# Performance work log

Hardware: AMD Instinct MI355X
Metric: run time of the kernel (lower is better)

The kernel has to match this reference:

```python
import jax, jax.numpy as jnp
import numpy as np

SEQ, DM, NH, DH = 8192, 1024, 16, 64


def setup_inputs() -> dict:
    key = jax.random.key(0)
    k = jax.random.split(key, 8)
    return {
        "xs": jax.random.normal(k[0], (SEQ, DM), dtype=jnp.float32),
        "wq": jax.random.normal(k[1], (NH, DH, DM), dtype=jnp.float32),
        "wk": jax.random.normal(k[2], (NH, DH, DM), dtype=jnp.float32),
        "wv": jax.random.normal(k[3], (NH, DH, DM), dtype=jnp.float32),
        # MLP: Linear(NH*DH -> DM), gelu, Linear(DM -> NH*DH); eqx stores W as (out, in)
        "w1": jax.random.normal(k[4], (DM, NH * DH), dtype=jnp.float32) * 0.02,
        "b1": jnp.zeros((DM,), dtype=jnp.float32),
        "w2": jax.random.normal(k[5], (NH * DH, DM), dtype=jnp.float32) * 0.02,
        "b2": jnp.zeros((NH * DH,), dtype=jnp.float32),
    }


def _act(x):
    return jax.nn.elu(x) + 1.0


def reference(xs, wq, wk, wv, w1, b1, w2, b2):
    # project: (n_heads d_head d_model),(seq d_model) -> (seq n_heads d_head)
    q = jnp.einsum('hdm,sm->shd', wq, xs)
    k = jnp.einsum('hdm,sm->shd', wk, xs)
    v = jnp.einsum('hdm,sm->shd', wv, xs)

    def cell(state, qkv):
        s, z = state                      # s: (h, dk, dv), z: (h, dk)
        qt, kt, vt = qkv                  # each (h, d)
        kt = _act(kt)
        s = s + jnp.einsum('hk,hv->hkv', kt, vt)
        z = z + kt
        qa = _act(qt)
        # faithful to einops 'n_heads d_head_k d_head_v, n_heads d_head_q -> n_heads d_head_v'
        sq = jnp.einsum('hkv,hq->hv', s, qa)
        zq = jnp.einsum('hk,hq->h', z, qa)
        return (s, z), sq / zq[:, None]

    init = (jnp.zeros((NH, DH, DH), xs.dtype), jnp.zeros((NH, DH), xs.dtype))
    _, out = jax.lax.scan(cell, init, (q, k, v))   # out: (seq, h, d)
    out = out.reshape(SEQ, NH * DH)
    h = jax.nn.gelu(out @ w1.T + b1)
    return h @ w2.T + b2
```

## Files before the change

kernel.cpp:

```cpp
#include <hip/hip_runtime.h>
#include <hip/hip_bf16.h>

using bf16 = __hip_bfloat16;
typedef __attribute__((ext_vector_type(8))) short shortx8;
typedef __attribute__((ext_vector_type(4))) float f32x4;

#define SEQ 8192
#define DM 1024
#define NH 16
#define CHUNK 64
#define NC (SEQ / CHUNK)
#define NT (DM / 64)

__device__ __forceinline__ void load_lds16(const bf16* g, bf16* l) {
    __builtin_amdgcn_global_load_lds(
        (const __attribute__((address_space(1))) void*)g,
        (__attribute__((address_space(3))) void*)l, 16, 0, 0);
}

__device__ __forceinline__ unsigned ldsoff(const bf16* p) {
    return (unsigned)(unsigned long long)(__attribute__((address_space(3))) const void*)p;
}

__device__ __forceinline__ shortx8 dsr128(unsigned a) {
    shortx8 r;
    asm volatile("ds_read_b128 %0, %1" : "=v"(r) : "v"(a));
    return r;
}

__device__ __forceinline__ float bf2f(short s) {
    union { unsigned u; float f; } x;
    x.u = ((unsigned)(unsigned short)s) << 16;
    return x.f;
}

__global__ __launch_bounds__(256) void convert_all(const float* __restrict__ xs,
                                                   const float* __restrict__ wk,
                                                   const float* __restrict__ wv,
                                                   const float* __restrict__ w1,
                                                   const float* __restrict__ w2,
                                                   bf16* __restrict__ xsb,
                                                   bf16* __restrict__ wall) {
    const int b = blockIdx.x;
    const float* in;
    bf16* out;
    int blk;
    if (b < 8192) {
        in = xs; out = xsb; blk = b;
    } else {
        const int seg = (b - 8192) >> 10;
        blk = (b - 8192) & 1023;
        out = wall + (size_t)seg * DM * DM;
        if (seg == 0)      in = wk;
        else if (seg == 1) in = wv;
        else if (seg == 2) in = w1;
        else               in = w2;
    }
    size_t i = ((size_t)blk * 256 + threadIdx.x) * 4;
    float4 f = *(const float4*)(in + i);
    out[i + 0] = __float2bfloat16(f.x);
    out[i + 1] = __float2bfloat16(f.y);
    out[i + 2] = __float2bfloat16(f.z);
    out[i + 3] = __float2bfloat16(f.w);
}

__global__ __launch_bounds__(512, 2) void gemm256(const bf16* __restrict__ A,
                                                  const bf16* __restrict__ B,
                                                  void* __restrict__ Cv,
                                                  float* __restrict__ kappa,
                                                  int N) {
    __shared__ __align__(16) bf16 As[2][256][64];
    __shared__ __align__(16) bf16 Bs[2][256][64];

    const int tid = threadIdx.x;
    const int nwg = gridDim.x * gridDim.y;
    const int bid = blockIdx.x + blockIdx.y * gridDim.x;
    const int cpx = nwg >> 3;
    const int swz = (bid & 7) * cpx + (bid >> 3);
    const int ry  = swz % gridDim.y;
    const int rx  = swz / gridDim.y;
    const int bm  = ry * 256;
    const int bn  = rx * 256;

    const int wave = tid >> 6;
    const int lane = tid & 63;
    const int wr   = wave >> 2;
    const int wc   = wave & 3;
    const int quad = lane >> 4;
    const int m16  = lane & 15;
    const int r7   = m16 & 7;
    const int wr128 = wr * 128;
    const int wc64  = wc * 64;
    const int kp0 = ((quad ^ r7) * 8);
    const int kp1 = (((4 + quad) ^ r7) * 8);

    auto stageA = [&](int half, int kt) {
        #pragma unroll
        for (int it = 0; it < 2; ++it) {
            int s = it * 512 + tid;
            int row = s >> 3, pos = s & 7;
            int g = pos ^ (row & 7);
            load_lds16(A + (size_t)(bm + half * 128 + row) * DM + kt * 64 + g * 8,
                       &As[kt & 1][half * 128 + row][pos * 8]);
        }
    };
    auto stageB = [&](int half, int kt) {
        #pragma unroll
        for (int it = 0; it < 2; ++it) {
            int s = it * 512 + tid;
            int row = s >> 3, pos = s & 7;
            int g = pos ^ (row & 7);
            load_lds16(B + (size_t)(bn + half * 128 + row) * DM + kt * 64 + g * 8,
                       &Bs[kt & 1][half * 128 + row][pos * 8]);
        }
    };

    f32x4 acc[8][4];
    #pragma unroll
    for (int i = 0; i < 8; ++i)
        #pragma unroll
        for (int j = 0; j < 4; ++j)
            #pragma unroll
            for (int r = 0; r < 4; ++r) acc[i][j][r] = 0.f;

    stageA(0, 0); stageA(1, 0); stageB(0, 0); stageB(1, 0);
    stageB(0, 1); stageB(1, 1);
    asm volatile("s_waitcnt vmcnt(4)");
    __builtin_amdgcn_s_barrier();

    shortx8 af[4][2], blo[2][2], bhi[2][2];

    #pragma unroll 1
    for (int t = 0; t < NT; ++t) {
        const int sl = t & 1;
        if (t + 1 < NT) { stageA(0, t + 1); stageA(1, t + 1); }
        #pragma unroll
        for (int i = 0; i < 4; ++i) {
            af[i][0] = dsr128(ldsoff(&As[sl][wr128 + i * 16 + m16][kp0]));
            af[i][1] = dsr128(ldsoff(&As[sl][wr128 + i * 16 + m16][kp1]));
        }
        #pragma unroll
        for (int j = 0; j < 2; ++j) {
            blo[j][0] = dsr128(ldsoff(&Bs[sl][wc64 + j * 16 + m16][kp0]));
            blo[j][1] = dsr128(ldsoff(&Bs[sl][wc64 + j * 16 + m16][kp1]));
            bhi[j][0] = dsr128(ldsoff(&Bs[sl][wc64 + (j + 2) * 16 + m16][kp0]));
            bhi[j][1] = dsr128(ldsoff(&Bs[sl][wc64 + (j + 2) * 16 + m16][kp1]));
        }
        asm volatile("s_waitcnt lgkmcnt(0)");
        __builtin_amdgcn_sched_barrier(0);
        __builtin_amdgcn_s_setprio(1);
        #pragma unroll
        for (int i = 0; i < 4; ++i)
            #pragma unroll
            for (int j = 0; j < 2; ++j) {
                acc[i][j] = __builtin_amdgcn_mfma_f32_16x16x32_bf16(af[i][0], blo[j][0], acc[i][j], 0, 0, 0);
                acc[i][j] = __builtin_amdgcn_mfma_f32_16x16x32_bf16(af[i][1], blo[j][1], acc[i][j], 0, 0, 0);
                acc[i][j + 2] = __builtin_amdgcn_mfma_f32_16x16x32_bf16(af[i][0], bhi[j][0], acc[i][j + 2], 0, 0, 0);
                acc[i][j + 2] = __builtin_amdgcn_mfma_f32_16x16x32_bf16(af[i][1], bhi[j][1], acc[i][j + 2], 0, 0, 0);
            }
        __builtin_amdgcn_s_setprio(0);
        __builtin_amdgcn_s_barrier();

        if (t + 2 < NT) { stageB(0, t + 2); stageB(1, t + 2); }
        #pragma unroll
        for (int i = 0; i < 4; ++i) {
            af[i][0] = dsr128(ldsoff(&As[sl][wr128 + 64 + i * 16 + m16][kp0]));
            af[i][1] = dsr128(ldsoff(&As[sl][wr128 + 64 + i * 16 + m16][kp1]));
        }
        asm volatile("s_waitcnt lgkmcnt(0)");
        __builtin_amdgcn_sched_barrier(0);
        __builtin_amdgcn_s_setprio(1);
        #pragma unroll
        for (int i = 0; i < 4; ++i)
            #pragma unroll
            for (int j = 0; j < 2; ++j) {
                acc[4 + i][j] = __builtin_amdgcn_mfma_f32_16x16x32_bf16(af[i][0], blo[j][0], acc[4 + i][j], 0, 0, 0);
                acc[4 + i][j] = __builtin_amdgcn_mfma_f32_16x16x32_bf16(af[i][1], blo[j][1], acc[4 + i][j], 0, 0, 0);
                acc[4 + i][j + 2] = __builtin_amdgcn_mfma_f32_16x16x32_bf16(af[i][0], bhi[j][0], acc[4 + i][j + 2], 0, 0, 0);
                acc[4 + i][j + 2] = __builtin_amdgcn_mfma_f32_16x16x32_bf16(af[i][1], bhi[j][1], acc[4 + i][j + 2], 0, 0, 0);
            }
        __builtin_amdgcn_s_setprio(0);
        if (t + 2 < NT) {
            asm volatile("s_waitcnt vmcnt(4)");
        } else {
            asm volatile("s_waitcnt vmcnt(0)");
        }
        __builtin_amdgcn_s_barrier();
    }

    const int gcol0 = bn + wc64;
    if (gcol0 < DM) {
        const int h = gcol0 >> 6;
        #pragma unroll
        for (int i = 0; i < 8; ++i) {
            #pragma unroll
            for (int r = 0; r < 4; ++r) {
                float s = 0.f;
                #pragma unroll
                for (int j = 0; j < 4; ++j) {
                    float v = acc[i][j][r];
                    s += v > 0.f ? v + 1.f : __expf(v);
                }
                s += __shfl_xor(s, 1);
                s += __shfl_xor(s, 2);
                s += __shfl_xor(s, 4);
                s += __shfl_xor(s, 8);
                if (m16 == 0)
                    kappa[(size_t)h * SEQ + bm + wr128 + i * 16 + quad * 4 + r] = s;
            }
        }
    } else {
        bf16* vb = (bf16*)Cv;
        #pragma unroll
        for (int i = 0; i < 8; ++i) {
            int row0 = bm + wr128 + i * 16 + quad * 4;
            #pragma unroll
            for (int j = 0; j < 4; ++j) {
                int col = gcol0 - DM + j * 16 + m16;
                #pragma unroll
                for (int r = 0; r < 4; ++r)
                    vb[(size_t)(row0 + r) * DM + col] = __float2bfloat16(acc[i][j][r]);
            }
        }
    }
}

template <int MODE>
__global__ __launch_bounds__(512, 2) void gemm_mlp(const bf16* __restrict__ A,
                                                   const bf16* __restrict__ B,
                                                   void* __restrict__ Cv,
                                                   const float* __restrict__ bias,
                                                   int N) {
    __shared__ __align__(16) bf16 As[3][128][64];
    __shared__ __align__(16) bf16 Bs[2][256][64];

    const int tid = threadIdx.x;
    const int nwg = gridDim.x * gridDim.y;
    const int bid = blockIdx.x + blockIdx.y * gridDim.x;
    const int cpx = nwg >> 3;
    const int swz = (bid & 7) * cpx + (bid >> 3);
    const int ry  = swz % gridDim.y;
    const int rx  = swz / gridDim.y;
    const int bm  = ry * 128;
    const int bn  = rx * 256;

    const int wave = tid >> 6;
    const int lane = tid & 63;
    const int wr   = wave >> 2;
    const int wc   = wave & 3;
    const int quad = lane >> 4;
    const int m16  = lane & 15;
    const int r7   = m16 & 7;
    const int wr64 = wr * 64;
    const int wc64 = wc * 64;
    const int kp0 = ((quad ^ r7) * 8);
    const int kp1 = (((4 + quad) ^ r7) * 8);

    auto stageA = [&](int slot, int kt) {
        #pragma unroll
        for (int it = 0; it < 2; ++it) {
            int s = it * 512 + tid;
            int row = s >> 3, pos = s & 7;
            int g = pos ^ (row & 7);
            load_lds16(A + (size_t)(bm + row) * DM + kt * 64 + g * 8,
                       &As[slot][row][pos * 8]);
        }
    };
    auto stageB = [&](int half, int kt) {
        #pragma unroll
        for (int it = 0; it < 2; ++it) {
            int s = it * 512 + tid;
            int row = s >> 3, pos = s & 7;
            int g = pos ^ (row & 7);
            load_lds16(B + (size_t)(bn + half * 128 + row) * DM + kt * 64 + g * 8,
                       &Bs[kt & 1][half * 128 + row][pos * 8]);
        }
    };

    f32x4 acc[4][4];
    #pragma unroll
    for (int i = 0; i < 4; ++i)
        #pragma unroll
        for (int j = 0; j < 4; ++j)
            #pragma unroll
            for (int r = 0; r < 4; ++r) acc[i][j][r] = 0.f;

    stageA(0, 0); stageB(0, 0); stageB(1, 0);
    stageA(1, 1); stageB(0, 1); stageB(1, 1);
    asm volatile("s_waitcnt vmcnt(6)");
    __builtin_amdgcn_s_barrier();

    shortx8 af[4][2], bfr[4][2];

    int sl3 = 0;
    int st3 = 2;

    #pragma unroll 1
    for (int t = 0; t < NT; ++t) {
        const int slB = t & 1;
        if (t + 2 < NT) stageA(st3, t + 2);
        #pragma unroll
        for (int i = 0; i < 4; ++i) {
            af[i][0] = dsr128(ldsoff(&As[sl3][wr64 + i * 16 + m16][kp0]));
            af[i][1] = dsr128(ldsoff(&As[sl3][wr64 + i * 16 + m16][kp1]));
        }
        #pragma unroll
        for (int j = 0; j < 4; ++j) {
            bfr[j][0] = dsr128(ldsoff(&Bs[slB][wc64 + j * 16 + m16][kp0]));
            bfr[j][1] = dsr128(ldsoff(&Bs[slB][wc64 + j * 16 + m16][kp1]));
        }
        asm volatile("s_waitcnt lgkmcnt(0)");
        __builtin_amdgcn_sched_barrier(0);
        __builtin_amdgcn_s_setprio(1);
        #pragma unroll
        for (int i = 0; i < 4; ++i)
            #pragma unroll
            for (int j = 0; j < 2; ++j) {
                acc[i][j] = __builtin_amdgcn_mfma_f32_16x16x32_bf16(af[i][0], bfr[j][0], acc[i][j], 0, 0, 0);
                acc[i][j] = __builtin_amdgcn_mfma_f32_16x16x32_bf16(af[i][1], bfr[j][1], acc[i][j], 0, 0, 0);
            }
        __builtin_amdgcn_s_setprio(0);
        __builtin_amdgcn_s_barrier();

        if (t + 2 < NT) { stageB(0, t + 2); stageB(1, t + 2); }
        __builtin_amdgcn_s_setprio(1);
        #pragma unroll
        for (int i = 0; i < 4; ++i)
            #pragma unroll
            for (int j = 0; j < 2; ++j) {
                acc[i][j + 2] = __builtin_amdgcn_mfma_f32_16x16x32_bf16(af[i][0], bfr[j + 2][0], acc[i][j + 2], 0, 0, 0);
                acc[i][j + 2] = __builtin_amdgcn_mfma_f32_16x16x32_bf16(af[i][1], bfr[j + 2][1], acc[i][j + 2], 0, 0, 0);
            }
        __builtin_amdgcn_s_setprio(0);
        if (t + 2 < NT) {
            asm volatile("s_waitcnt vmcnt(6)");
        } else {
            asm volatile("s_waitcnt vmcnt(0)");
        }
        __builtin_amdgcn_s_barrier();
        sl3 = (sl3 == 2) ? 0 : sl3 + 1;
        st3 = (st3 == 2) ? 0 : st3 + 1;
    }

    #pragma unroll
    for (int i = 0; i < 4; ++i) {
        int row0 = bm + wr64 + i * 16 + quad * 4;
        #pragma unroll
        for (int j = 0; j < 4; ++j) {
            int col = bn + wc64 + j * 16 + m16;
            float bv = bias[col];
            #pragma unroll
            for (int r = 0; r < 4; ++r) {
                float v = acc[i][j][r] + bv;
                if (MODE == 2) {
                    float tt = tanhf(0.7978845608028654f * (v + 0.044715f * v * v * v));
                    ((bf16*)Cv)[(size_t)(row0 + r) * N + col] = __float2bfloat16(0.5f * v * (1.f + tt));
                } else {
                    ((float*)Cv)[(size_t)(row0 + r) * N + col] = v;
                }
            }
        }
    }
}

__global__ __launch_bounds__(256) void chunk_sums(const bf16* __restrict__ vb,
                                                  const float* __restrict__ kappa,
                                                  float* __restrict__ numbuf,
                                                  float* __restrict__ denbuf) {
    const int h = blockIdx.x, c = blockIdx.y;
    const int v = threadIdx.x & 63, tq = threadIdx.x >> 6;
    __shared__ float red[4][64];
    __shared__ float dred[4];
    float np = 0.f, dp = 0.f;
    #pragma unroll
    for (int i = 0; i < 16; ++i) {
        int t = c * 64 + tq * 16 + i;
        float kv = kappa[(size_t)h * SEQ + t];
        float vv = bf2f(((const short*)vb)[(size_t)t * DM + h * 64 + v]);
        np += kv * vv;
        dp += kv;
    }
    red[tq][v] = np;
    if (v == 0) dred[tq] = dp;
    __syncthreads();
    if (tq == 0) {
        float s = red[0][v] + red[1][v] + red[2][v] + red[3][v];
        numbuf[((size_t)h * NC + c) * 64 + v] = s;
        if (v == 0)
            denbuf[(size_t)h * NC + c] = dred[0] + dred[1] + dred[2] + dred[3];
    }
}

__global__ __launch_bounds__(256) void prefix_state(float* __restrict__ numbuf,
                                                    float* __restrict__ denbuf) {
    const int h = blockIdx.x;
    const int wave = threadIdx.x >> 6;
    const int d = threadIdx.x & 63;
    __shared__ float tot[4][64];
    __shared__ float dtot[4];

    float val[32], dval[32];
    const int c0 = wave * 32;
    #pragma unroll
    for (int i = 0; i < 32; ++i) {
        size_t idx = (size_t)h * NC + c0 + i;
        val[i]  = numbuf[idx * 64 + d];
        dval[i] = denbuf[idx];
    }
    float run = 0.f, drun = 0.f;
    #pragma unroll
    for (int i = 0; i < 32; ++i) {
        float t = val[i];  val[i]  = run;  run  += t;
        float dt = dval[i]; dval[i] = drun; drun += dt;
    }
    tot[wave][d] = run;
    if (d == 0) dtot[wave] = drun;
    __syncthreads();
    float off = 0.f, doff = 0.f;
    for (int w = 0; w < wave; ++w) { off += tot[w][d]; doff += dtot[w]; }
    #pragma unroll
    for (int i = 0; i < 32; ++i) {
        size_t idx = (size_t)h * NC + c0 + i;
        numbuf[idx * 64 + d] = val[i] + off;
        if (d == 0) denbuf[idx] = dval[i] + doff;
    }
}

__global__ __launch_bounds__(256) void chunk_out(const bf16* __restrict__ vb,
                                                 const float* __restrict__ kappa,
                                                 const float* __restrict__ numbuf,
                                                 const float* __restrict__ denbuf,
                                                 bf16* __restrict__ out) {
    const int h = blockIdx.x, c = blockIdx.y;
    __shared__ float Ksh[64];
    __shared__ float Vs[64][64];
    const int tid = threadIdx.x;

    #pragma unroll
    for (int it = 0; it < 2; ++it) {
        int s = it * 256 + tid;
        int r = s >> 3, d8 = (s & 7) * 8;
        shortx8 raw = *(const shortx8*)(vb + (size_t)(c * 64 + r) * DM + h * 64 + d8);
        #pragma unroll
        for (int e = 0; e < 8; ++e) Vs[r][d8 + e] = bf2f(raw[e]);
    }
    if (tid < 64) Ksh[tid] = kappa[(size_t)h * SEQ + c * 64 + tid];
    __syncthreads();

    const int t  = tid >> 2;
    const int v0 = (tid & 3) << 4;
    const size_t bidx = (size_t)h * NC + c;

    float den = denbuf[bidx];
    float num[16];
    #pragma unroll
    for (int jj = 0; jj < 4; ++jj) {
        float4 n4 = *(const float4*)&numbuf[bidx * 64 + v0 + jj * 4];
        num[jj * 4 + 0] = n4.x; num[jj * 4 + 1] = n4.y;
        num[jj * 4 + 2] = n4.z; num[jj * 4 + 3] = n4.w;
    }

    for (int i = 0; i <= t; ++i) {
        float s = Ksh[i];
        den += s;
        #pragma unroll
        for (int jj = 0; jj < 4; ++jj) {
            float4 v4 = *(const float4*)&Vs[i][v0 + jj * 4];
            num[jj * 4 + 0] += s * v4.x; num[jj * 4 + 1] += s * v4.y;
            num[jj * 4 + 2] += s * v4.z; num[jj * 4 + 3] += s * v4.w;
        }
    }

    const float inv = 1.0f / den;
    size_t og = (size_t)(c * 64 + t) * DM + h * 64 + v0;
    #pragma unroll
    for (int j = 0; j < 16; ++j) out[og + j] = __float2bfloat16(num[j] * inv);
}

extern "C" void kernel_launch(void* const* d_in, const int* in_sizes, int n_in,
                              void* d_out, int out_size, void* d_ws, size_t ws_size,
                              hipStream_t stream) {
    const float* xs = (const float*)d_in[0];
    const float* wk = (const float*)d_in[2];
    const float* wv = (const float*)d_in[3];
    const float* w1 = (const float*)d_in[4];
    const float* b1 = (const float*)d_in[5];
    const float* w2 = (const float*)d_in[6];
    const float* b2 = (const float*)d_in[7];
    float* y = (float*)d_out;

    char* base = (char*)d_ws;
    size_t off = 0;
    auto alloc = [&](size_t b) -> char* {
        char* p = base + off;
        off += (b + 255) & ~(size_t)255;
        return p;
    };

    const size_t NMAT = (size_t)SEQ * DM;
    const size_t NW   = (size_t)DM * DM;
    bf16*  xsb    = (bf16*)alloc(NMAT * 2);
    bf16*  wall   = (bf16*)alloc(4 * NW * 2);
    bf16*  w1b    = wall + 2 * NW;
    bf16*  w2b    = wall + 3 * NW;
    bf16*  vb     = (bf16*)alloc(NMAT * 2);
    float* kappa  = (float*)alloc((size_t)NH * SEQ * 4);
    float* numbuf = (float*)alloc((size_t)NH * NC * 64 * 4);
    float* denbuf = (float*)alloc((size_t)NH * NC * 4);
    bf16*  outb   = (bf16*)alloc(NMAT * 2);
    bf16*  hb     = (bf16*)alloc(NMAT * 2);

    convert_all<<<8192 + 4 * 1024, 256, 0, stream>>>(xs, wk, wv, w1, w2,
                                                     xsb, wall);

    gemm256<<<dim3(2048 / 256, SEQ / 256), 512, 0, stream>>>(
        xsb, wall, vb, kappa, 2048);

    chunk_sums<<<dim3(NH, NC), 256, 0, stream>>>(vb, kappa, numbuf, denbuf);
    prefix_state<<<NH, 256, 0, stream>>>(numbuf, denbuf);
    chunk_out<<<dim3(NH, NC), 256, 0, stream>>>(vb, kappa, numbuf, denbuf, outb);

    gemm_mlp<2><<<dim3(DM / 256, SEQ / 128), 512, 0, stream>>>(
        outb, w1b, hb, b1, DM);
    gemm_mlp<3><<<dim3(DM / 256, SEQ / 128), 512, 0, stream>>>(
        hb, w2b, y, b2, DM);
}
```

Baseline: 215.4 us.

## Replace quadratic intra-chunk output with per-lane sequential scan using wave shuffles

The chunk-output kernel is replaced. It used to stage V in LDS and have each thread redo a prefix sum over up to 64 rows (quadratic work). Now each wave owns one chunk and each lane owns one value column, so the running numerator and denominator are updated in one sequential pass, with kappa broadcast by shuffles. The chunk-sum kernel is reorganised the same way, one wave per chunk, with a shuffle reduction for the denominator, removing the LDS reductions and barriers. The new pattern does 2-byte strided loads and stores per lane across rows and a divide per step, and the launch uses a quarter as many blocks.

```diff
diff --git a/kernel.cpp b/kernel.cpp
--- a/kernel.cpp
+++ b/kernel.cpp
@@ -367,27 +367,51 @@
                                                   const float* __restrict__ kappa,
                                                   float* __restrict__ numbuf,
                                                   float* __restrict__ denbuf) {
-    const int h = blockIdx.x, c = blockIdx.y;
-    const int v = threadIdx.x & 63, tq = threadIdx.x >> 6;
-    __shared__ float red[4][64];
-    __shared__ float dred[4];
-    float np = 0.f, dp = 0.f;
-    #pragma unroll
-    for (int i = 0; i < 16; ++i) {
-        int t = c * 64 + tq * 16 + i;
-        float kv = kappa[(size_t)h * SEQ + t];
-        float vv = bf2f(((const short*)vb)[(size_t)t * DM + h * 64 + v]);
-        np += kv * vv;
-        dp += kv;
-    }
-    red[tq][v] = np;
-    if (v == 0) dred[tq] = dp;
-    __syncthreads();
-    if (tq == 0) {
-        float s = red[0][v] + red[1][v] + red[2][v] + red[3][v];
-        numbuf[((size_t)h * NC + c) * 64 + v] = s;
-        if (v == 0)
-            denbuf[(size_t)h * NC + c] = dred[0] + dred[1] + dred[2] + dred[3];
+    const int h = blockIdx.x;
+    const int c = blockIdx.y * 4 + (threadIdx.x >> 6);
+    const int v = threadIdx.x & 63;
+    const size_t bidx = (size_t)h * NC + c;
+
+    float kreg = kappa[(size_t)h * SEQ + c * 64 + v];
+    float num = 0.f;
+    const short* vrow = (const short*)vb + (size_t)(c * 64) * DM + h * 64 + v;
+    #pragma unroll 8
+    for (int t = 0; t < 64; ++t) {
+        float kt = __shfl(kreg, t);
+        num += kt * bf2f(vrow[0]);
+        vrow += DM;
+    }
+    numbuf[bidx * 64 + v] = num;
+    float d = kreg;
+    #pragma unroll
+    for (int off = 32; off > 0; off >>= 1) d += __shfl_xor(d, off);
+    if (v == 0) denbuf[bidx] = d;
+}
+
+__global__ __launch_bounds__(256) void chunk_scan(const bf16* __restrict__ vb,
+                                                  const float* __restrict__ kappa,
+                                                  const float* __restrict__ numbuf,
+                                                  const float* __restrict__ denbuf,
+                                                  bf16* __restrict__ out) {
+    const int h = blockIdx.x;
+    const int c = blockIdx.y * 4 + (threadIdx.x >> 6);
+    const int v = threadIdx.x & 63;
+    const size_t bidx = (size_t)h * NC + c;
+
+    float kreg = kappa[(size_t)h * SEQ + c * 64 + v];
+    float num = numbuf[bidx * 64 + v];
+    float den = denbuf[bidx];
+    const short* vrow = (const short*)vb + (size_t)(c * 64) * DM + h * 64 + v;
+    short* orow = (short*)out + (size_t)(c * 64) * DM + h * 64 + v;
+    #pragma unroll 8
+    for (int t = 0; t < 64; ++t) {
+        float kt = __shfl(kreg, t);
+        num += kt * bf2f(vrow[0]);
+        den += kt;
+        bf16 ob = __float2bfloat16(num / den);
+        orow[0] = *(const short*)&ob;
+        vrow += DM;
+        orow += DM;
     }
 }
 
@@ -424,57 +448,6 @@
         numbuf[idx * 64 + d] = val[i] + off;
         if (d == 0) denbuf[idx] = dval[i] + doff;
     }
-}
-
-__global__ __launch_bounds__(256) void chunk_out(const bf16* __restrict__ vb,
-                                                 const float* __restrict__ kappa,
-                                                 const float* __restrict__ numbuf,
-                                                 const float* __restrict__ denbuf,
-                                                 bf16* __restrict__ out) {
-    const int h = blockIdx.x, c = blockIdx.y;
-    __shared__ float Ksh[64];
-    __shared__ float Vs[64][64];
-    const int tid = threadIdx.x;
-
-    #pragma unroll
-    for (int it = 0; it < 2; ++it) {
-        int s = it * 256 + tid;
-        int r = s >> 3, d8 = (s & 7) * 8;
-        shortx8 raw = *(const shortx8*)(vb + (size_t)(c * 64 + r) * DM + h * 64 + d8);
-        #pragma unroll
-        for (int e = 0; e < 8; ++e) Vs[r][d8 + e] = bf2f(raw[e]);
-    }
-    if (tid < 64) Ksh[tid] = kappa[(size_t)h * SEQ + c * 64 + tid];
-    __syncthreads();
-
-    const int t  = tid >> 2;
-    const int v0 = (tid & 3) << 4;
-    const size_t bidx = (size_t)h * NC + c;
-
-    float den = denbuf[bidx];
-    float num[16];
-    #pragma unroll
-    for (int jj = 0; jj < 4; ++jj) {
-        float4 n4 = *(const float4*)&numbuf[bidx * 64 + v0 + jj * 4];
-        num[jj * 4 + 0] = n4.x; num[jj * 4 + 1] = n4.y;
-        num[jj * 4 + 2] = n4.z; num[jj * 4 + 3] = n4.w;
-    }
-
-    for (int i = 0; i <= t; ++i) {
-        float s = Ksh[i];
-        den += s;
-        #pragma unroll
-        for (int jj = 0; jj < 4; ++jj) {
-            float4 v4 = *(const float4*)&Vs[i][v0 + jj * 4];
-            num[jj * 4 + 0] += s * v4.x; num[jj * 4 + 1] += s * v4.y;
-            num[jj * 4 + 2] += s * v4.z; num[jj * 4 + 3] += s * v4.w;
-        }
-    }
-
-    const float inv = 1.0f / den;
-    size_t og = (size_t)(c * 64 + t) * DM + h * 64 + v0;
-    #pragma unroll
-    for (int j = 0; j < 16; ++j) out[og + j] = __float2bfloat16(num[j] * inv);
 }
 
 extern "C" void kernel_launch(void* const* d_in, const int* in_sizes, int n_in,
@@ -516,9 +489,10 @@
     gemm256<<<dim3(2048 / 256, SEQ / 256), 512, 0, stream>>>(
         xsb, wall, vb, kappa, 2048);
 
-    chunk_sums<<<dim3(NH, NC), 256, 0, stream>>>(vb, kappa, numbuf, denbuf);
+    chunk_sums<<<dim3(NH, NC / 4), 256, 0, stream>>>(vb, kappa, numbuf, denbuf);
     prefix_state<<<NH, 256, 0, stream>>>(numbuf, denbuf);
-    chunk_out<<<dim3(NH, NC), 256, 0, stream>>>(vb, kappa, numbuf, denbuf, outb);
+    chunk_scan<<<dim3(NH, NC / 4), 256, 0, stream>>>(vb, kappa, numbuf, denbuf,
+                                                     outb);
 
     gemm_mlp<2><<<dim3(DM / 256, SEQ / 128), 512, 0, stream>>>(
         outb, w1b, hb, b1, DM);
```

After: 205.9 us, median of 4. 4.4% less time.
